# Optimization experiments

Hardware: AMD Instinct MI355X
Metric: run time of the kernel (lower is better)

The kernel has to match this reference:

```python
import jax, jax.numpy as jnp
import numpy as np

N_NODES = 50000
N_EDGES = 800000
D = 64
N_LAYERS = 3
N_AGG = 4   # mean, max, min, std
N_SC = 3    # identity, amplification, attenuation
DELTA = float(np.log(17.0))  # `deg` init arg = avg log-degree normalizer
SLOPE = 0.01                 # leaky_relu default negative slope


def setup_inputs() -> dict:
    key = jax.random.key(0)
    ks = jax.random.split(key, 6)
    h = jax.random.normal(ks[0], (N_NODES, D), jnp.float32)
    src = jax.random.randint(ks[1], (N_EDGES,), 0, N_NODES, jnp.int32)
    dst = jax.random.randint(ks[2], (N_EDGES,), 0, N_NODES, jnp.int32)
    u_in = (N_AGG * N_SC + 1) * D  # 13*D input to U
    M_w = jax.random.normal(ks[3], (N_LAYERS, D, 2 * D), jnp.float32) / np.sqrt(2 * D)
    M_b = jnp.zeros((N_LAYERS, D), jnp.float32)
    U_w = jax.random.normal(ks[4], (N_LAYERS, D, u_in), jnp.float32) / np.sqrt(u_in)
    U_b = jnp.zeros((N_LAYERS, D), jnp.float32)
    mix_w = jax.random.normal(ks[5], (N_LAYERS, D, D), jnp.float32) / np.sqrt(D)
    mix_b = jnp.zeros((N_LAYERS, D), jnp.float32)
    return dict(h=h, src=src, dst=dst, M_w=M_w, M_b=M_b,
                U_w=U_w, U_b=U_b, mix_w=mix_w, mix_b=mix_b)


def _pna_layer(h, src, dst, mw, mb, uw, ub, xw, xb):
    n = h.shape[0]
    # per-edge message: leaky_relu(M([h_src || h_dst]))
    f = jnp.concatenate([h[src], h[dst]], axis=-1)        # [E, 2D]
    msg = jax.nn.leaky_relu(f @ mw.T + mb, SLOPE)         # [E, D]
    # degree-bucketed multi-aggregation via segment reductions
    deg = jax.ops.segment_sum(jnp.ones((msg.shape[0],), h.dtype), dst, num_segments=n)
    degc = jnp.maximum(deg, 1.0)[:, None]                 # avoid /0 for isolated nodes
    s = jax.ops.segment_sum(msg, dst, num_segments=n)
    ssq = jax.ops.segment_sum(msg * msg, dst, num_segments=n)
    mean = s / degc
    var = jax.nn.relu(ssq / degc - mean * mean)
    std = jnp.sqrt(var + 1e-30)
    has = (deg > 0)[:, None]
    mx = jnp.where(has, jax.ops.segment_max(msg, dst, num_segments=n), 0.0)
    mn = jnp.where(has, jax.ops.segment_min(msg, dst, num_segments=n), 0.0)
    std = jnp.where(has, std, 0.0)
    agg = jnp.concatenate([mean, mx, mn, std], axis=-1)   # [N, 4D]
    # scalers: identity, amplification, attenuation
    logd = jnp.log(jnp.maximum(deg, 1.0) + 1.0)[:, None]
    scaled = jnp.concatenate([agg, agg * (logd / DELTA), agg * (DELTA / logd)], axis=-1)  # [N, 12D]
    out = jnp.concatenate([h, scaled], axis=-1) @ uw.T + ub   # U: [N, D]
    out = jax.nn.leaky_relu(out @ xw.T + xb, SLOPE)           # mixing layer
    return out + h                                             # residual (in==out)


def reference(h, src, dst, M_w, M_b, U_w, U_b, mix_w, mix_b):
    h = jnp.round(h * 100.0) / 100.0
    for i in range(N_LAYERS):
        h = _pna_layer(h, src, dst, M_w[i], M_b[i], U_w[i], U_b[i], mix_w[i], mix_b[i])
        h = jax.nn.relu(h)
    return jnp.sum(h, axis=0, keepdims=True)  # SumPooling over single graph -> [1, D]
```

## Files before the change

### kernel.cpp

```cpp
#include <hip/hip_runtime.h>

#define NN 50000
#define EE 800000
#define DD 64
#define NL 3
#define UIN 832
#define XW 256
#define DELTA_F 2.833213344056216f
#define SLOPE 0.01f
#define SCAN_BLKS 196
#define UPD_BLKS 512
#define NTILE 3125
#define SHP 80

typedef __attribute__((ext_vector_type(8))) short short8;
typedef __attribute__((ext_vector_type(4))) float floatx4;

__device__ __align__(16) unsigned short g_hb[2][NN * DD];
__device__ __align__(16) unsigned short g_p1[NN * DD];
__device__ __align__(16) unsigned short g_p2[NN * DD];
__device__ __align__(16) unsigned short g_x2[NN * XW];
__device__ __align__(16) float          g_sc[NN * 2];
__device__ __align__(16) unsigned short g_BfragU[NL * 26 * 4 * 512];
__device__ __align__(16) unsigned short g_BfragM[NL * 4 * 4 * 512];
__device__ float g_bcomb[NL * DD];
__device__ int   g_cnt[NN];
__device__ int   g_roff[NN + 1];
__device__ __align__(16) unsigned short g_csrc[EE];
__device__ __align__(16) unsigned short g_epos[EE];
__device__ int   g_bsum[SCAN_BLKS], g_boff[SCAN_BLKS];

__device__ __forceinline__ float bf2f(unsigned short u) {
  return __uint_as_float(((unsigned)u) << 16);
}
__device__ __forceinline__ unsigned short f2bf(float f) {
  unsigned u = __float_as_uint(f);
  return (unsigned short)((u + 0x7FFFu + ((u >> 16) & 1u)) >> 16);
}
__device__ __forceinline__ float lrelu(float x) { return fmaxf(x, x * SLOPE); }

__global__ void __launch_bounds__(256) k_zero() {
  int i = blockIdx.x * 256 + threadIdx.x;
  if (i < NN) g_cnt[i] = 0;
}

__global__ void __launch_bounds__(256) k_prephist(const float* __restrict__ h,
                                                  const int* __restrict__ dst) {
  int i = blockIdx.x * 256 + threadIdx.x;
  if (i < NN * DD) {
    float v = rintf(h[i] * 100.f) / 100.f;
    g_hb[0][i] = f2bf(v);
  }
  if (i < EE) {
    int d = dst[i];
    int p = atomicAdd(&g_cnt[d], 1);
    g_epos[i] = (unsigned short)p;
  }
}

__global__ void __launch_bounds__(256) k_scan_a() {
  __shared__ int sh[256];
  int t = threadIdx.x;
  int idx = blockIdx.x * 256 + t;
  sh[t] = (idx < NN) ? g_cnt[idx] : 0;
  __syncthreads();
  for (int off = 128; off > 0; off >>= 1) {
    if (t < off) sh[t] += sh[t + off];
    __syncthreads();
  }
  if (t == 0) g_bsum[blockIdx.x] = sh[0];
}

__global__ void __launch_bounds__(256) k_scan_b() {
  __shared__ int sh[256];
  int t = threadIdx.x;
  sh[t] = (t < SCAN_BLKS) ? g_bsum[t] : 0;
  __syncthreads();
  for (int off = 1; off < 256; off <<= 1) {
    int v = (t >= off) ? sh[t - off] : 0;
    __syncthreads();
    sh[t] += v;
    __syncthreads();
  }
  if (t < SCAN_BLKS) g_boff[t] = (t == 0) ? 0 : sh[t - 1];
}

__global__ void __launch_bounds__(256) k_scan_c() {
  __shared__ int sh[256];
  int t = threadIdx.x;
  int idx = blockIdx.x * 256 + t;
  int v = (idx < NN) ? g_cnt[idx] : 0;
  sh[t] = v;
  __syncthreads();
  for (int off = 1; off < 256; off <<= 1) {
    int x = (t >= off) ? sh[t - off] : 0;
    __syncthreads();
    sh[t] += x;
    __syncthreads();
  }
  if (idx < NN) g_roff[idx] = g_boff[blockIdx.x] + sh[t] - v;
  if (blockIdx.x == 0 && t == 0) g_roff[NN] = EE;
}

__global__ void __launch_bounds__(256) k_scatter(const int* __restrict__ src,
                                                 const int* __restrict__ dst) {
  int i = blockIdx.x * 256 + threadIdx.x;
  if (i < EE) {
    int d = dst[i];
    g_csrc[g_roff[d] + (int)g_epos[i]] = (unsigned short)src[i];
  }
}

__global__ void __launch_bounds__(256) k_weights(const float* __restrict__ Uw,
                                                 const float* __restrict__ mixw,
                                                 const float* __restrict__ Mw,
                                                 const float* __restrict__ Ub,
                                                 const float* __restrict__ mixb) {
  int idx = blockIdx.x * 256 + threadIdx.x;
  if (idx < NL * DD * UIN) {
    int l = idx / (DD * UIN);
    int rem = idx - l * (DD * UIN);
    int d = rem / UIN;
    int k = rem - d * UIN;
    const float* xw = mixw + (l * DD + d) * DD;
    const float* uc = Uw + (size_t)l * DD * UIN + k;
    float s = 0.f;
    for (int j = 0; j < DD; ++j) s += xw[j] * uc[(size_t)j * UIN];
    int kt = k >> 5, kr = k & 31, g = kr >> 3, j8 = kr & 7, nb = d >> 4;
    int ln = (g << 4) | (d & 15);
    g_BfragU[(((l * 26 + kt) * 4 + nb) << 9) + ln * 8 + j8] = f2bf(s);
  }
  if (idx < NL * DD * 128) {
    int l = idx >> 13;
    int rem = idx & 8191;
    int d = rem >> 7;
    int k = rem & 127;
    float w = Mw[idx];
    int kt = k >> 5, kr = k & 31, g = kr >> 3, j8 = kr & 7, nb = d >> 4;
    int ln = (g << 4) | (d & 15);
    g_BfragM[(((l * 4 + kt) * 4 + nb) << 9) + ln * 8 + j8] = f2bf(w);
  }
  if (idx < NL * DD) {
    int l = idx >> 6, d = idx & 63;
    const float* xw = mixw + (l * DD + d) * DD;
    const float* ub = Ub + l * DD;
    float s = 0.f;
    for (int j = 0; j < DD; ++j) s += xw[j] * ub[j];
    g_bcomb[idx] = s + mixb[idx];
  }
}

__global__ void __launch_bounds__(256, 2) k_pre(const float* __restrict__ Mb,
                                                int L, int par) {
  int lane = threadIdx.x & 63;
  int nb = threadIdx.x >> 6;
  int chunk = (lane >> 4) << 3;
  const unsigned short* bp = g_BfragM + (size_t)L * 16 * 512;
  short8 B1[2], B2[2];
#pragma unroll
  for (int kt = 0; kt < 2; ++kt) {
    B1[kt] = *(const short8*)(bp + ((kt * 4 + nb) << 9) + lane * 8);
    B2[kt] = *(const short8*)(bp + (((kt + 2) * 4 + nb) << 9) + lane * 8);
  }
  float mb = Mb[L * DD + nb * 16 + (lane & 15)];
  const unsigned short* hb = g_hb[par];

  for (int wt = blockIdx.x; wt < NTILE; wt += gridDim.x) {
    int rowA = wt * 16 + (lane & 15);
    const unsigned short* hp = hb + (size_t)rowA * DD;
    floatx4 a1, a2;
#pragma unroll
    for (int r = 0; r < 4; ++r) { a1[r] = 0.f; a2[r] = 0.f; }
#pragma unroll
    for (int kt = 0; kt < 2; ++kt) {
      short8 a = *(const short8*)(hp + kt * 32 + chunk);
      a1 = __builtin_amdgcn_mfma_f32_16x16x32_bf16(a, B1[kt], a1, 0, 0, 0);
      a2 = __builtin_amdgcn_mfma_f32_16x16x32_bf16(a, B2[kt], a2, 0, 0, 0);
    }
#pragma unroll
    for (int r = 0; r < 4; ++r) {
      int row = wt * 16 + 4 * (lane >> 4) + r;
      int col = nb * 16 + (lane & 15);
      g_p1[row * DD + col] = f2bf(a1[r]);
      g_p2[row * DD + col] = f2bf(a2[r] + mb);
    }
  }
}

#define AGG_PROC(v)                                              \
  {                                                              \
    float lo = __uint_as_float((v) << 16) + b0;                  \
    float hi = __uint_as_float((v) & 0xffff0000u) + b1;          \
    lo = fmaxf(lo, lo * SLOPE);                                  \
    hi = fmaxf(hi, hi * SLOPE);                                  \
    s0 += lo; q0 += lo * lo; mx0 = fmaxf(mx0, lo); mn0 = fminf(mn0, lo); \
    s1 += hi; q1 += hi * hi; mx1 = fmaxf(mx1, hi); mn1 = fminf(mn1, hi); \
  }

__global__ void __launch_bounds__(256) k_aggf() {
  int lane = threadIdx.x & 63;
  int n = blockIdx.x * 4 + (threadIdx.x >> 6);
  int r0 = g_roff[n], r1 = g_roff[n + 1];
  int p = lane >> 5;
  int c2 = lane & 31;
  const unsigned* p1u = (const unsigned*)g_p1;
  const unsigned* p2u = (const unsigned*)g_p2;
  unsigned pv = p2u[(size_t)n * 32 + c2];
  float b0 = __uint_as_float(pv << 16);
  float b1 = __uint_as_float(pv & 0xffff0000u);
  float s0 = 0.f, q0 = 0.f, mx0 = -3.4e38f, mn0 = 3.4e38f;
  float s1 = 0.f, q1 = 0.f, mx1 = -3.4e38f, mn1 = 3.4e38f;
  for (int base = r0; base < r1; base += 64) {
    int m = min(64, r1 - base);
    int sv = (lane < m) ? (int)g_csrc[base + lane] : 0;
    int j = p;
    for (; j + 6 < m; j += 8) {
      int sn0 = __shfl(sv, j);
      int sn1 = __shfl(sv, j + 2);
      int sn2 = __shfl(sv, j + 4);
      int sn3 = __shfl(sv, j + 6);
      unsigned v0 = p1u[(size_t)sn0 * 32 + c2];
      unsigned v1 = p1u[(size_t)sn1 * 32 + c2];
      unsigned v2 = p1u[(size_t)sn2 * 32 + c2];
      unsigned v3 = p1u[(size_t)sn3 * 32 + c2];
      AGG_PROC(v0); AGG_PROC(v1); AGG_PROC(v2); AGG_PROC(v3);
    }
    for (; j < m; j += 2) {
      int sn = __shfl(sv, j);
      unsigned v = p1u[(size_t)sn * 32 + c2];
      AGG_PROC(v);
    }
  }
  s0 += __shfl_xor(s0, 32); q0 += __shfl_xor(q0, 32);
  mx0 = fmaxf(mx0, __shfl_xor(mx0, 32)); mn0 = fminf(mn0, __shfl_xor(mn0, 32));
  s1 += __shfl_xor(s1, 32); q1 += __shfl_xor(q1, 32);
  mx1 = fmaxf(mx1, __shfl_xor(mx1, 32)); mn1 = fminf(mn1, __shfl_xor(mn1, 32));

  int deg = r1 - r0;
  float degc = fmaxf((float)deg, 1.f);
  float mean0 = s0 / degc, mean1 = s1 / degc;
  unsigned* xp = (unsigned*)(g_x2 + (size_t)n * XW);
  if (p == 0) {
    if (deg == 0) { mx0 = 0.f; mx1 = 0.f; }
    xp[c2]      = (unsigned)f2bf(mean0) | ((unsigned)f2bf(mean1) << 16);
    xp[32 + c2] = (unsigned)f2bf(mx0)   | ((unsigned)f2bf(mx1)   << 16);
    if (c2 == 0) {
      float logd = logf(degc + 1.f);
      g_sc[n * 2] = logd / DELTA_F;
      g_sc[n * 2 + 1] = DELTA_F / logd;
    }
  } else {
    float sd0 = sqrtf(fmaxf(q0 / degc - mean0 * mean0, 0.f) + 1e-30f);
    float sd1 = sqrtf(fmaxf(q1 / degc - mean1 * mean1, 0.f) + 1e-30f);
    if (deg == 0) { mn0 = 0.f; mn1 = 0.f; sd0 = 0.f; sd1 = 0.f; }
    xp[64 + c2] = (unsigned)f2bf(mn0)   | ((unsigned)f2bf(mn1)   << 16);
    xp[96 + c2] = (unsigned)f2bf(sd0)   | ((unsigned)f2bf(sd1)   << 16);
  }
}

__global__ void __launch_bounds__(256, 2) k_update(int L, int par,
                                                   const float* __restrict__ Mb,
                                                   float* __restrict__ out) {
  __shared__ __align__(16) unsigned short sh[16 * SHP];
  int lane = threadIdx.x & 63;
  int nb = threadIdx.x >> 6;
  int chunk = (lane >> 4) << 3;
  const unsigned short* bp = g_BfragU + (size_t)L * 26 * 4 * 512;

  short8 Bf[26];
#pragma unroll
  for (int i = 0; i < 26; ++i)
    Bf[i] = *(const short8*)(bp + ((i * 4 + nb) << 9) + lane * 8);
  float bc = g_bcomb[L * DD + nb * 16 + (lane & 15)];
  int Lp = (L < 2) ? L + 1 : 2;
  const unsigned short* mp = g_BfragM + (size_t)Lp * 16 * 512;
  short8 B1[2], B2[2];
#pragma unroll
  for (int kt = 0; kt < 2; ++kt) {
    B1[kt] = *(const short8*)(mp + ((kt * 4 + nb) << 9) + lane * 8);
    B2[kt] = *(const short8*)(mp + (((kt + 2) * 4 + nb) << 9) + lane * 8);
  }
  float mb2 = Mb[Lp * DD + nb * 16 + (lane & 15)];
  const unsigned short* hb = g_hb[par];
  unsigned short* hbn = g_hb[par ^ 1];

  float csum = 0.f;
  for (int wt = blockIdx.x; wt < NTILE; wt += gridDim.x) {
    int rbase = wt * 16;
    int rowA = rbase + (lane & 15);
    const unsigned short* hp = hb + (size_t)rowA * DD;
    const unsigned short* ap = g_x2 + (size_t)rowA * XW;
    floatx4 acc0, acc2, acc3;
#pragma unroll
    for (int r = 0; r < 4; ++r) { acc0[r] = 0.f; acc2[r] = 0.f; acc3[r] = 0.f; }
#pragma unroll
    for (int kk = 0; kk < 10; ++kk) {
      short8 a = (kk < 2) ? *(const short8*)(hp + kk * 32 + chunk)
                          : *(const short8*)(ap + (kk - 2) * 32 + chunk);
      acc0 = __builtin_amdgcn_mfma_f32_16x16x32_bf16(a, Bf[kk], acc0, 0, 0, 0);
    }
#pragma unroll
    for (int kk = 0; kk < 8; ++kk) {
      short8 a = *(const short8*)(ap + kk * 32 + chunk);
      acc2 = __builtin_amdgcn_mfma_f32_16x16x32_bf16(a, Bf[10 + kk], acc2, 0, 0, 0);
      acc3 = __builtin_amdgcn_mfma_f32_16x16x32_bf16(a, Bf[18 + kk], acc3, 0, 0, 0);
    }
#pragma unroll
    for (int r = 0; r < 4; ++r) {
      int row_l = 4 * (lane >> 4) + r;
      int row = rbase + row_l;
      float s1 = g_sc[row * 2], s2 = g_sc[row * 2 + 1];
      int col = nb * 16 + (lane & 15);
      float y = lrelu(acc0[r] + s1 * acc2[r] + s2 * acc3[r] + bc);
      float hn = fmaxf(y + bf2f(hb[row * DD + col]), 0.f);
      unsigned short h16 = f2bf(hn);
      hbn[row * DD + col] = h16;
      sh[row_l * SHP + col] = h16;
      csum += hn;
    }
    __syncthreads();
    if (L < 2) {
      floatx4 a1, a2;
#pragma unroll
      for (int r = 0; r < 4; ++r) { a1[r] = 0.f; a2[r] = 0.f; }
#pragma unroll
      for (int kt = 0; kt < 2; ++kt) {
        short8 a = *(const short8*)(sh + (lane & 15) * SHP + kt * 32 + chunk);
        a1 = __builtin_amdgcn_mfma_f32_16x16x32_bf16(a, B1[kt], a1, 0, 0, 0);
        a2 = __builtin_amdgcn_mfma_f32_16x16x32_bf16(a, B2[kt], a2, 0, 0, 0);
      }
#pragma unroll
      for (int r = 0; r < 4; ++r) {
        int row = rbase + 4 * (lane >> 4) + r;
        int col = nb * 16 + (lane & 15);
        g_p1[row * DD + col] = f2bf(a1[r]);
        g_p2[row * DD + col] = f2bf(a2[r] + mb2);
      }
    }
    __syncthreads();
  }
  if (L == 2) {
    csum += __shfl_xor(csum, 16);
    csum += __shfl_xor(csum, 32);
    if ((lane >> 4) == 0) atomicAdd(out + nb * 16 + lane, csum);
  }
}

extern "C" void kernel_launch(void* const* d_in, const int* in_sizes, int n_in,
                              void* d_out, int out_size, void* d_ws, size_t ws_size,
                              hipStream_t stream) {
  const float* h    = (const float*)d_in[0];
  const int*   src  = (const int*)d_in[1];
  const int*   dst  = (const int*)d_in[2];
  const float* Mw   = (const float*)d_in[3];
  const float* Mb   = (const float*)d_in[4];
  const float* Uw   = (const float*)d_in[5];
  const float* Ub   = (const float*)d_in[6];
  const float* mixw = (const float*)d_in[7];
  const float* mixb = (const float*)d_in[8];
  float* out = (float*)d_out;

  hipMemsetAsync(out, 0, (size_t)out_size * sizeof(float), stream);

  k_zero<<<196, 256, 0, stream>>>();
  k_prephist<<<12500, 256, 0, stream>>>(h, dst);
  k_scan_a<<<SCAN_BLKS, 256, 0, stream>>>();
  k_scan_b<<<1, 256, 0, stream>>>();
  k_scan_c<<<SCAN_BLKS, 256, 0, stream>>>();
  k_scatter<<<3125, 256, 0, stream>>>(src, dst);
  k_weights<<<624, 256, 0, stream>>>(Uw, mixw, Mw, Ub, mixb);

  k_pre<<<UPD_BLKS, 256, 0, stream>>>(Mb, 0, 0);
  for (int L = 0; L < NL; ++L) {
    int par = L & 1;
    k_aggf<<<12500, 256, 0, stream>>>();
    k_update<<<UPD_BLKS, 256, 0, stream>>>(L, par, Mb, out);
  }
}
```

Baseline: 276.6 us.

## Assign one node per half-wave in aggregation and double update grid

The aggregation kernel now maps each 32-lane half-wave to its own destination node, so every wave handles two nodes instead of splitting one node's edges across both halves. This drops the cross-half shuffle reduction and the divergent per-half write paths, and halves the aggregation grid size. The update and pre kernels also launch twice as many blocks. The trade-off is worse load balance: the two nodes in a wave can have different degrees, so lanes may idle while waiting on the longer edge list.

```diff
diff --git a/kernel.cpp b/kernel.cpp
--- a/kernel.cpp
+++ b/kernel.cpp
@@ -9,7 +9,7 @@
 #define DELTA_F 2.833213344056216f
 #define SLOPE 0.01f
 #define SCAN_BLKS 196
-#define UPD_BLKS 512
+#define UPD_BLKS 1024
 #define NTILE 3125
 #define SHP 80
 
@@ -199,10 +199,11 @@
 
 __global__ void __launch_bounds__(256) k_aggf() {
   int lane = threadIdx.x & 63;
-  int n = blockIdx.x * 4 + (threadIdx.x >> 6);
+  int wid = threadIdx.x >> 6;
+  int c2 = lane & 31;
+  int hbase = lane & 32;
+  int n = blockIdx.x * 8 + wid * 2 + (lane >> 5);
   int r0 = g_roff[n], r1 = g_roff[n + 1];
-  int p = lane >> 5;
-  int c2 = lane & 31;
   const unsigned* p1u = (const unsigned*)g_p1;
   const unsigned* p2u = (const unsigned*)g_p2;
   unsigned pv = p2u[(size_t)n * 32 + c2];
@@ -210,51 +211,42 @@
   float b1 = __uint_as_float(pv & 0xffff0000u);
   float s0 = 0.f, q0 = 0.f, mx0 = -3.4e38f, mn0 = 3.4e38f;
   float s1 = 0.f, q1 = 0.f, mx1 = -3.4e38f, mn1 = 3.4e38f;
-  for (int base = r0; base < r1; base += 64) {
-    int m = min(64, r1 - base);
-    int sv = (lane < m) ? (int)g_csrc[base + lane] : 0;
-    int j = p;
-    for (; j + 6 < m; j += 8) {
-      int sn0 = __shfl(sv, j);
-      int sn1 = __shfl(sv, j + 2);
-      int sn2 = __shfl(sv, j + 4);
-      int sn3 = __shfl(sv, j + 6);
+  for (int base = r0; base < r1; base += 32) {
+    int m = min(32, r1 - base);
+    int sv = (c2 < m) ? (int)g_csrc[base + c2] : 0;
+    int j = 0;
+    for (; j + 3 < m; j += 4) {
+      int sn0 = __shfl(sv, hbase + j);
+      int sn1 = __shfl(sv, hbase + j + 1);
+      int sn2 = __shfl(sv, hbase + j + 2);
+      int sn3 = __shfl(sv, hbase + j + 3);
       unsigned v0 = p1u[(size_t)sn0 * 32 + c2];
       unsigned v1 = p1u[(size_t)sn1 * 32 + c2];
       unsigned v2 = p1u[(size_t)sn2 * 32 + c2];
       unsigned v3 = p1u[(size_t)sn3 * 32 + c2];
       AGG_PROC(v0); AGG_PROC(v1); AGG_PROC(v2); AGG_PROC(v3);
     }
-    for (; j < m; j += 2) {
-      int sn = __shfl(sv, j);
+    for (; j < m; ++j) {
+      int sn = __shfl(sv, hbase + j);
       unsigned v = p1u[(size_t)sn * 32 + c2];
       AGG_PROC(v);
     }
   }
-  s0 += __shfl_xor(s0, 32); q0 += __shfl_xor(q0, 32);
-  mx0 = fmaxf(mx0, __shfl_xor(mx0, 32)); mn0 = fminf(mn0, __shfl_xor(mn0, 32));
-  s1 += __shfl_xor(s1, 32); q1 += __shfl_xor(q1, 32);
-  mx1 = fmaxf(mx1, __shfl_xor(mx1, 32)); mn1 = fminf(mn1, __shfl_xor(mn1, 32));
-
   int deg = r1 - r0;
   float degc = fmaxf((float)deg, 1.f);
   float mean0 = s0 / degc, mean1 = s1 / degc;
+  float sd0 = sqrtf(fmaxf(q0 / degc - mean0 * mean0, 0.f) + 1e-30f);
+  float sd1 = sqrtf(fmaxf(q1 / degc - mean1 * mean1, 0.f) + 1e-30f);
+  if (deg == 0) { mx0 = 0.f; mx1 = 0.f; mn0 = 0.f; mn1 = 0.f; sd0 = 0.f; sd1 = 0.f; }
   unsigned* xp = (unsigned*)(g_x2 + (size_t)n * XW);
-  if (p == 0) {
-    if (deg == 0) { mx0 = 0.f; mx1 = 0.f; }
-    xp[c2]      = (unsigned)f2bf(mean0) | ((unsigned)f2bf(mean1) << 16);
-    xp[32 + c2] = (unsigned)f2bf(mx0)   | ((unsigned)f2bf(mx1)   << 16);
-    if (c2 == 0) {
-      float logd = logf(degc + 1.f);
-      g_sc[n * 2] = logd / DELTA_F;
-      g_sc[n * 2 + 1] = DELTA_F / logd;
-    }
-  } else {
-    float sd0 = sqrtf(fmaxf(q0 / degc - mean0 * mean0, 0.f) + 1e-30f);
-    float sd1 = sqrtf(fmaxf(q1 / degc - mean1 * mean1, 0.f) + 1e-30f);
-    if (deg == 0) { mn0 = 0.f; mn1 = 0.f; sd0 = 0.f; sd1 = 0.f; }
-    xp[64 + c2] = (unsigned)f2bf(mn0)   | ((unsigned)f2bf(mn1)   << 16);
-    xp[96 + c2] = (unsigned)f2bf(sd0)   | ((unsigned)f2bf(sd1)   << 16);
+  xp[c2]      = (unsigned)f2bf(mean0) | ((unsigned)f2bf(mean1) << 16);
+  xp[32 + c2] = (unsigned)f2bf(mx0)   | ((unsigned)f2bf(mx1)   << 16);
+  xp[64 + c2] = (unsigned)f2bf(mn0)   | ((unsigned)f2bf(mn1)   << 16);
+  xp[96 + c2] = (unsigned)f2bf(sd0)   | ((unsigned)f2bf(sd1)   << 16);
+  if (c2 == 0) {
+    float logd = logf(degc + 1.f);
+    g_sc[n * 2] = logd / DELTA_F;
+    g_sc[n * 2 + 1] = DELTA_F / logd;
   }
 }
 
@@ -373,7 +365,7 @@
   k_pre<<<UPD_BLKS, 256, 0, stream>>>(Mb, 0, 0);
   for (int L = 0; L < NL; ++L) {
     int par = L & 1;
-    k_aggf<<<12500, 256, 0, stream>>>();
+    k_aggf<<<6250, 256, 0, stream>>>();
     k_update<<<UPD_BLKS, 256, 0, stream>>>(L, par, Mb, out);
   }
 }
```

Result: faster. 268.9 us (-2.8%).
